# Performance work log

Measured on AMD Instinct MI355X. Metric: run time of the kernel, lower is better.

## Reference

```python
import jax, jax.numpy as jnp
import numpy as np

NUM_LABELS = 10  # number of distinct label values in the minibatch
EPS = 1e-8


def setup_inputs() -> dict:
    key = jax.random.key(0)
    k1, k2 = jax.random.split(key)
    z = jax.random.normal(k1, (8192, 20, 256), dtype=jnp.float32)  # [B, C, H]
    labels = jax.random.randint(k2, (8192,), 0, NUM_LABELS)  # [B]
    return {"z": z, "labels": labels}


def reference(z, labels):
    # CODI minibatch loss, positive pairs, representation space.
    # Equivalent to: for each unique label, mse(z[group] + 1e-8, mean(z[group]))
    # summed over labels. Vectorized as a single segment-mean +
    # gather-broadcast + segment-SSE pass (one traversal of z).
    z = jnp.nan_to_num(z)
    B, C, H = z.shape
    counts = jax.ops.segment_sum(
        jnp.ones((B,), dtype=z.dtype), labels, num_segments=NUM_LABELS
    )  # [K]
    sums = jax.ops.segment_sum(z, labels, num_segments=NUM_LABELS)  # [K, C, H]
    means = jnp.nan_to_num(sums / jnp.maximum(counts, 1.0)[:, None, None])
    # per-sample squared distance to its group's mean (note the +EPS as in torch)
    d = (z + EPS) - means[labels]  # [B, C, H]
    per_sample = jnp.sum(d * d, axis=(1, 2))  # [B]
    sse = jax.ops.segment_sum(per_sample, labels, num_segments=NUM_LABELS)  # [K]
    # nn.MSELoss is a mean over all elements of the group: count_k * C * H
    mse_k = sse / (jnp.maximum(counts, 1.0) * (C * H))
    # torch.unique only visits labels present in the batch -> mask empty groups
    return jnp.sum(jnp.where(counts > 0, jnp.nan_to_num(mse_k), 0.0))
```

## Files before the change

### kernel.cpp

```cpp
#include <hip/hip_runtime.h>

#define B_SZ   8192
#define CH     5120
#define CH4    1280
#define K_LAB  10
#define EPS    1e-8f
#define FLTMAX 3.402823466e38f

#define NTHR   256
#define NCHUNK 5
#define PS     16
#define PF     8


__global__ __launch_bounds__(640) void codi_setup(
    const int* __restrict__ labels, int* __restrict__ idx,
    int* __restrict__ off, float* __restrict__ SSQ, float* __restrict__ nsq)
{
    const int tid  = threadIdx.x;
    const int k    = tid >> 6;
    const int lane = tid & 63;
    __shared__ int cnts[K_LAB];
    __shared__ int offs[K_LAB + 1];

    int cnt = 0;
    for (int b0 = 0; b0 < B_SZ; b0 += 64) {
        int lab = labels[b0 + lane];
        cnt += __popcll(__ballot(lab == k));
    }
    if (lane == 0) cnts[k] = cnt;
    __syncthreads();
    if (tid == 0) {
        int a = 0;
        for (int j = 0; j < K_LAB; ++j) { offs[j] = a; a += cnts[j]; }
        offs[K_LAB] = a;
    }
    __syncthreads();

    int base = offs[k];
    const unsigned long long ltmask = (1ULL << lane) - 1ULL;
    for (int b0 = 0; b0 < B_SZ; b0 += 64) {
        int lab = labels[b0 + lane];
        unsigned long long m = __ballot(lab == k);
        if (lab == k) idx[base + __popcll(m & ltmask)] = b0 + lane;
        base += __popcll(m);
    }
    if (tid < K_LAB + 1) off[tid] = offs[tid];
    if (tid < K_LAB) { SSQ[tid] = 0.f; nsq[tid] = 0.f; }
}

__global__ __launch_bounds__(NTHR) void codi_gather(
    const float4* __restrict__ z4, const int* __restrict__ idx,
    const int* __restrict__ off, float4* __restrict__ S_part,
    float* __restrict__ SSQ)
{
    const int tid   = threadIdx.x;
    const int k     = blockIdx.x / (NCHUNK * PS);
    const int rem   = blockIdx.x % (NCHUNK * PS);
    const int chunk = rem % NCHUNK;
    const int ps    = rem / NCHUNK;

    const int kb  = off[k];
    const int cnt = off[k + 1] - kb;
    const int s0  = kb + (int)(((long long)cnt * ps) / PS);
    const int s1  = kb + (int)(((long long)cnt * (ps + 1)) / PS);
    const int n   = s1 - s0;

    __shared__ int rows[544];
    for (int i = tid; i < n; i += NTHR) rows[i] = idx[s0 + i];
    __syncthreads();

    const int col4 = chunk * NTHR + tid;
    float4 sum = make_float4(0.f, 0.f, 0.f, 0.f);
    float  ssq = 0.f;

    for (int i0 = 0; i0 < n; i0 += PF) {
        int r[PF];
        #pragma unroll
        for (int u = 0; u < PF; ++u)
            if (i0 + u < n) r[u] = rows[i0 + u];

        float4 vb[PF];
        #pragma unroll
        for (int u = 0; u < PF; ++u)
            if (i0 + u < n) vb[u] = z4[(size_t)r[u] * CH4 + col4];

        #pragma unroll
        for (int u = 0; u < PF; ++u) {
            if (i0 + u < n) {
                float4 v = vb[u];
                v.x = (v.x == v.x) ? fminf(fmaxf(v.x, -FLTMAX), FLTMAX) : 0.f;
                v.y = (v.y == v.y) ? fminf(fmaxf(v.y, -FLTMAX), FLTMAX) : 0.f;
                v.z = (v.z == v.z) ? fminf(fmaxf(v.z, -FLTMAX), FLTMAX) : 0.f;
                v.w = (v.w == v.w) ? fminf(fmaxf(v.w, -FLTMAX), FLTMAX) : 0.f;
                sum.x += v.x; sum.y += v.y; sum.z += v.z; sum.w += v.w;
                ssq = fmaf(v.x, v.x, ssq); ssq = fmaf(v.y, v.y, ssq);
                ssq = fmaf(v.z, v.z, ssq); ssq = fmaf(v.w, v.w, ssq);
            }
        }
    }

    S_part[((size_t)(k * PS + ps)) * CH4 + col4] = sum;

    #pragma unroll
    for (int o = 32; o > 0; o >>= 1) ssq += __shfl_down(ssq, o, 64);
    if ((tid & 63) == 0) atomicAdd(&SSQ[k], ssq);
}

__global__ __launch_bounds__(NTHR) void codi_reduce(
    const float* __restrict__ S_part, float* __restrict__ nsq)
{
    const int i = blockIdx.x * NTHR + threadIdx.x;
    const int k = i / CH;
    const int c = i - k * CH;
    float s = 0.f;
    #pragma unroll
    for (int ps = 0; ps < PS; ++ps)
        s += S_part[((size_t)(k * PS + ps)) * CH + c];
    float w = s * s;
    #pragma unroll
    for (int o = 32; o > 0; o >>= 1) w += __shfl_down(w, o, 64);
    if ((threadIdx.x & 63) == 0) atomicAdd(&nsq[k], w);
}

__global__ __launch_bounds__(64) void codi_final(
    const int* __restrict__ off, const float* __restrict__ SSQ,
    const float* __restrict__ nsq, float* __restrict__ out)
{
    if (threadIdx.x == 0) {
        float loss = 0.f;
        for (int k = 0; k < K_LAB; ++k) {
            float n = (float)(off[k + 1] - off[k]);
            if (n > 0.f) {
                float sse = SSQ[k] - nsq[k] / n + n * (float)CH * (EPS * EPS);
                float mse = sse / (n * (float)CH);
                if (mse == mse) loss += mse;
            }
        }
        out[0] = loss;
    }
}

extern "C" void kernel_launch(void* const* d_in, const int* in_sizes, int n_in,
                              void* d_out, int out_size, void* d_ws, size_t ws_size,
                              hipStream_t stream) {
    const float4* z4     = (const float4*)d_in[0];
    const int*    labels = (const int*)d_in[1];

    float* hdr    = (float*)d_ws;
    float* SSQ    = hdr;
    float* nsq    = hdr + 16;
    int*   off    = (int*)(hdr + 32);
    int*   idx    = (int*)(hdr + 64);
    float* S_part = hdr + 64 + B_SZ;

    codi_setup<<<1, 640, 0, stream>>>(labels, idx, off, SSQ, nsq);
    codi_gather<<<K_LAB * NCHUNK * PS, NTHR, 0, stream>>>(
        z4, idx, off, (float4*)S_part, SSQ);
    codi_reduce<<<(K_LAB * CH) / NTHR, NTHR, 0, stream>>>(S_part, nsq);
    codi_final<<<1, 64, 0, stream>>>(off, SSQ, nsq, (float*)d_out);
}
```

Baseline: 298.9 us.

## Double gather partitions, stage labels in LDS, and peel unpredicated main loop

Doubles the number of sample partitions per label in the gather kernel (PS 16→32), so 1600 blocks instead of 800 stream z, each with fewer rows. The setup kernel now copies labels into shared memory once with vector loads instead of reading global memory twice per wave. The gather loop is split into an unpredicated main loop over full groups of 8 rows plus a guarded tail, removing per-element bounds checks. The costs are a reduce kernel that sums twice as many partial rows and a larger partial-sum buffer.

Result: no change. 301.2 us (+0.8%).

```diff
diff --git a/kernel.cpp b/kernel.cpp
--- a/kernel.cpp
+++ b/kernel.cpp
@@ -9,7 +9,7 @@
 
 #define NTHR   256
 #define NCHUNK 5
-#define PS     16
+#define PS     32
 #define PF     8
 
 
@@ -17,17 +17,20 @@
     const int* __restrict__ labels, int* __restrict__ idx,
     int* __restrict__ off, float* __restrict__ SSQ, float* __restrict__ nsq)
 {
+    __shared__ int lab_s[B_SZ];
+    __shared__ int cnts[K_LAB];
+    __shared__ int offs[K_LAB + 1];
     const int tid  = threadIdx.x;
     const int k    = tid >> 6;
     const int lane = tid & 63;
-    __shared__ int cnts[K_LAB];
-    __shared__ int offs[K_LAB + 1];
+
+    const int4* l4 = (const int4*)labels;
+    for (int i = tid; i < B_SZ / 4; i += 640) ((int4*)lab_s)[i] = l4[i];
+    __syncthreads();
 
     int cnt = 0;
-    for (int b0 = 0; b0 < B_SZ; b0 += 64) {
-        int lab = labels[b0 + lane];
-        cnt += __popcll(__ballot(lab == k));
-    }
+    for (int b0 = 0; b0 < B_SZ; b0 += 64)
+        cnt += __popcll(__ballot(lab_s[b0 + lane] == k));
     if (lane == 0) cnts[k] = cnt;
     __syncthreads();
     if (tid == 0) {
@@ -40,7 +43,7 @@
     int base = offs[k];
     const unsigned long long ltmask = (1ULL << lane) - 1ULL;
     for (int b0 = 0; b0 < B_SZ; b0 += 64) {
-        int lab = labels[b0 + lane];
+        int lab = lab_s[b0 + lane];
         unsigned long long m = __ballot(lab == k);
         if (lab == k) idx[base + __popcll(m & ltmask)] = b0 + lane;
         base += __popcll(m);
@@ -66,7 +69,7 @@
     const int s1  = kb + (int)(((long long)cnt * (ps + 1)) / PS);
     const int n   = s1 - s0;
 
-    __shared__ int rows[544];
+    __shared__ int rows[288];
     for (int i = tid; i < n; i += NTHR) rows[i] = idx[s0 + i];
     __syncthreads();
 
@@ -74,31 +77,38 @@
     float4 sum = make_float4(0.f, 0.f, 0.f, 0.f);
     float  ssq = 0.f;
 
-    for (int i0 = 0; i0 < n; i0 += PF) {
-        int r[PF];
-        #pragma unroll
-        for (int u = 0; u < PF; ++u)
-            if (i0 + u < n) r[u] = rows[i0 + u];
+#define SANITIZE(v) do { \
+        v.x = (v.x == v.x) ? fminf(fmaxf(v.x, -FLTMAX), FLTMAX) : 0.f; \
+        v.y = (v.y == v.y) ? fminf(fmaxf(v.y, -FLTMAX), FLTMAX) : 0.f; \
+        v.z = (v.z == v.z) ? fminf(fmaxf(v.z, -FLTMAX), FLTMAX) : 0.f; \
+        v.w = (v.w == v.w) ? fminf(fmaxf(v.w, -FLTMAX), FLTMAX) : 0.f; \
+    } while (0)
+#define ACCUM(v) do { \
+        sum.x += v.x; sum.y += v.y; sum.z += v.z; sum.w += v.w; \
+        ssq = fmaf(v.x, v.x, ssq); ssq = fmaf(v.y, v.y, ssq); \
+        ssq = fmaf(v.z, v.z, ssq); ssq = fmaf(v.w, v.w, ssq); \
+    } while (0)
 
+    const int n_main = n & ~(PF - 1);
+    for (int i0 = 0; i0 < n_main; i0 += PF) {
         float4 vb[PF];
         #pragma unroll
         for (int u = 0; u < PF; ++u)
-            if (i0 + u < n) vb[u] = z4[(size_t)r[u] * CH4 + col4];
-
+            vb[u] = z4[(size_t)rows[i0 + u] * CH4 + col4];
         #pragma unroll
-        for (int u = 0; u < PF; ++u) {
-            if (i0 + u < n) {
-                float4 v = vb[u];
-                v.x = (v.x == v.x) ? fminf(fmaxf(v.x, -FLTMAX), FLTMAX) : 0.f;
-                v.y = (v.y == v.y) ? fminf(fmaxf(v.y, -FLTMAX), FLTMAX) : 0.f;
-                v.z = (v.z == v.z) ? fminf(fmaxf(v.z, -FLTMAX), FLTMAX) : 0.f;
-                v.w = (v.w == v.w) ? fminf(fmaxf(v.w, -FLTMAX), FLTMAX) : 0.f;
-                sum.x += v.x; sum.y += v.y; sum.z += v.z; sum.w += v.w;
-                ssq = fmaf(v.x, v.x, ssq); ssq = fmaf(v.y, v.y, ssq);
-                ssq = fmaf(v.z, v.z, ssq); ssq = fmaf(v.w, v.w, ssq);
-            }
-        }
+        for (int u = 0; u < PF; ++u) { SANITIZE(vb[u]); ACCUM(vb[u]); }
     }
+    if (n_main < n) {
+        float4 vb[PF];
+        #pragma unroll
+        for (int u = 0; u < PF; ++u)
+            if (n_main + u < n) vb[u] = z4[(size_t)rows[n_main + u] * CH4 + col4];
+        #pragma unroll
+        for (int u = 0; u < PF; ++u)
+            if (n_main + u < n) { SANITIZE(vb[u]); ACCUM(vb[u]); }
+    }
+#undef SANITIZE
+#undef ACCUM
 
     S_part[((size_t)(k * PS + ps)) * CH4 + col4] = sum;
 
```
